# Kernel tuning notes

Measured on AMD Instinct MI355X. Metric: run time of the kernel, lower is better.

The kernel has to match this reference:

```python
import jax, jax.numpy as jnp
import numpy as np

B, S, HID = 2, 1024, 4096
NH, NKV = 32, 8            # query heads, kv heads (GQA)
D = HID // NH              # head_size = 128
G = NH // NKV              # groups = 4
SCALE = D ** -0.5


def setup_inputs() -> dict:
    key = jax.random.key(0)
    k1, k2, k3 = jax.random.split(key, 3)
    hidden_states = jax.random.normal(k1, (B, S, HID), dtype=jnp.float32)
    # rotary tables: dim=head_size, base=10000 (PositionRotaryEmbedding.static)
    inv_freq = 1.0 / (10000.0 ** (jnp.arange(0, D, 2, dtype=jnp.float32) / D))  # [D/2]
    t = jnp.arange(S, dtype=jnp.float32)
    freqs = jnp.outer(t, inv_freq)                       # [S, D/2]
    cos, sin = jnp.cos(freqs), jnp.sin(freqs)
    wqkv = jax.random.normal(k2, (HID, (NH + 2 * NKV) * D), dtype=jnp.float32) * (HID ** -0.5)
    wo = jax.random.normal(k3, (NH * D, HID), dtype=jnp.float32) * (HID ** -0.5)
    return {"hidden_states": hidden_states, "cos": cos, "sin": sin, "wqkv": wqkv, "wo": wo}


def _rope(x, cos, sin):
    # interleaved-pair rotary (TGI convention); x: [B,S,H,D], cos/sin: [S,D/2]
    x1, x2 = x[..., 0::2], x[..., 1::2]
    c = cos[None, :, None, :]
    s = sin[None, :, None, :]
    r1 = x1 * c - x2 * s
    r2 = x1 * s + x2 * c
    return jnp.stack([r1, r2], axis=-1).reshape(x.shape)


def reference(hidden_states, cos, sin, wqkv, wo):
    qkv = hidden_states @ wqkv                                  # [B,S,(NH+2*NKV)*D]
    q = qkv[..., : NH * D].reshape(B, S, NH, D)
    k = qkv[..., NH * D : (NH + NKV) * D].reshape(B, S, NKV, D)
    v = qkv[..., (NH + NKV) * D :].reshape(B, S, NKV, D)
    q = _rope(q, cos, sin)
    k = _rope(k, cos, sin)
    # GQA: group query heads over kv heads
    qg = q.reshape(B, S, NKV, G, D)
    scores = jnp.einsum('bqkgd,bskd->bkgqs', qg, k) * SCALE     # [B,NKV,G,S,S]
    causal = jnp.tril(jnp.ones((S, S), dtype=bool))
    scores = jnp.where(causal, scores, jnp.finfo(scores.dtype).min)
    p = jax.nn.softmax(scores, axis=-1)
    out = jnp.einsum('bkgqs,bskd->bqkgd', p, v).reshape(B, S, NH * D)
    return out @ wo                                             # [B,S,HID]
```

## Files before the change

kernel.cpp:

```cpp
#include <hip/hip_runtime.h>
#include <hip/hip_bf16.h>

typedef __bf16 bf16;
typedef __attribute__((ext_vector_type(2))) __bf16 bf16x2;
typedef __attribute__((ext_vector_type(4))) __bf16 bf16x4;
typedef __attribute__((ext_vector_type(8))) __bf16 bf16x8;
typedef __attribute__((ext_vector_type(4))) float f32x4;

#define NB 2
#define SEQ 1024
#define HIDN 4096
#define NH 32
#define NKV 8
#define DH 128
#define QKV_N 6144
static constexpr float SCALE = 0.08838834764831845f;

#define MFMA(a, b, c) __builtin_amdgcn_mfma_f32_16x16x32_bf16((a), (b), (c), 0, 0, 0)

__device__ __forceinline__ void async16(const void* g, void* l) {
  __builtin_amdgcn_global_load_lds(
      (const __attribute__((address_space(1))) unsigned int*)g,
      (__attribute__((address_space(3))) unsigned int*)l,
      16, 0, 0);
}

__device__ __forceinline__ void barrier_raw() {
  asm volatile("" ::: "memory");
  __builtin_amdgcn_s_barrier();
  asm volatile("" ::: "memory");
}
#define VMCNT(n) asm volatile("s_waitcnt vmcnt(" #n ")" ::: "memory")
#define LGKM0 asm volatile("s_waitcnt lgkmcnt(0)" ::: "memory")

__global__ __launch_bounds__(256) void cvt_f32_bf16(const float* __restrict__ src,
                                                    bf16* __restrict__ dst, int n4) {
  int i = blockIdx.x * 256 + threadIdx.x;
  if (i >= n4) return;
  const float4 v = ((const float4*)src)[i];
  bf16x4 o = {(bf16)v.x, (bf16)v.y, (bf16)v.z, (bf16)v.w};
  ((bf16x4*)dst)[i] = o;
}

__global__ __launch_bounds__(512) void transpose_cvt(const float* __restrict__ src,
                                                     bf16* __restrict__ dst, int R, int C) {
  __shared__ float tl[128][68];
  const int j0 = blockIdx.x * 64, i0 = blockIdx.y * 128;
  {
    const int r = threadIdx.x >> 2, c = (threadIdx.x & 3) * 16;
    const float* S = src + (size_t)(i0 + r) * C + j0 + c;
#pragma unroll
    for (int e = 0; e < 4; ++e) *(float4*)&tl[r][c + e * 4] = *(const float4*)&S[e * 4];
  }
  __syncthreads();
  {
    const int j = threadIdx.x >> 3, ic = (threadIdx.x & 7) * 16;
    bf16x8 o0, o1;
#pragma unroll
    for (int e = 0; e < 8; ++e) {
      o0[e] = (bf16)tl[ic + e][j];
      o1[e] = (bf16)tl[ic + 8 + e][j];
    }
    bf16* D = dst + (size_t)(j0 + j) * R + i0 + ic;
    *(bf16x8*)&D[0] = o0;
    *(bf16x8*)&D[8] = o1;
  }
}

__global__ __launch_bounds__(256) void vtrans(const bf16* __restrict__ src,
                                              bf16* __restrict__ dst) {
  __shared__ bf16 tl[64][72];
  const int bk = blockIdx.z;
  const int s0 = blockIdx.x * 64, d0 = blockIdx.y * 64;
  const bf16* S = src + ((size_t)bk * SEQ + s0) * DH + d0;
  bf16* D = dst + ((size_t)bk * DH + d0) * SEQ + s0;
  const int r = threadIdx.x >> 2, c = (threadIdx.x & 3) * 16;
  *(bf16x8*)&tl[r][c] = *(const bf16x8*)&S[(size_t)r * DH + c];
  *(bf16x8*)&tl[r][c + 8] = *(const bf16x8*)&S[(size_t)r * DH + c + 8];
  __syncthreads();
  bf16x8 o0, o1;
#pragma unroll
  for (int e = 0; e < 8; ++e) {
    o0[e] = tl[c + e][r];
    o1[e] = tl[c + 8 + e][r];
  }
  *(bf16x8*)&D[(size_t)r * SEQ + c] = o0;
  *(bf16x8*)&D[(size_t)r * SEQ + c + 8] = o1;
}

template <int BN, int MODE>
__global__ __launch_bounds__(512, 2) void gemm_dp(const bf16* __restrict__ A,
                                                  const bf16* __restrict__ BT,
                                                  void* __restrict__ Cout,
                                                  int N, int K,
                                                  const float* __restrict__ cosp,
                                                  const float* __restrict__ sinp,
                                                  bf16* __restrict__ Qo,
                                                  bf16* __restrict__ Ko,
                                                  bf16* __restrict__ Vo) {
  extern __shared__ char smem[];
  constexpr int CA = 128 * 32 * 2;
  constexpr int CB = BN * 32 * 2;
  constexpr int BUF = CA + CB;
  constexpr int LTOT = 1 + BN / 128;
  constexpr int FN = BN / 64;
  constexpr int FNH = FN / 2;
  const int t = threadIdx.x, lane = t & 63, w = t >> 6;
  const int l16 = lane & 15, lq = lane >> 4;
  const int wm = w >> 2, wn = w & 3;

  const int nwg = gridDim.x;
  const int lin = ((int)blockIdx.x & 7) * (nwg >> 3) + ((int)blockIdx.x >> 3);
  const int m0 = (lin & 15) * 128;
  const int n0 = (lin >> 4) * BN;

  const int sslot = (t & 3) ^ ((t >> 3) & 3);
  const bf16* gsrc[LTOT];
  gsrc[0] = A + (size_t)(m0 + (t >> 2)) * K + sslot * 8;
#pragma unroll
  for (int u = 1; u < LTOT; ++u)
    gsrc[u] = BT + (size_t)(n0 + (u - 1) * 128 + (t >> 2)) * K + sslot * 8;

  int abyte[4], bbyte[FN];
#pragma unroll
  for (int f = 0; f < 4; ++f) {
    const int r = wm * 64 + f * 16 + l16;
    abyte[f] = r * 64 + ((lq ^ ((r >> 1) & 3)) << 4);
  }
#pragma unroll
  for (int j = 0; j < FN; ++j) {
    const int r = wn * (BN / 4) + j * 16 + l16;
    bbyte[j] = CA + r * 64 + ((lq ^ ((r >> 1) & 3)) << 4);
  }

  auto stage_unit = [&](int kt, int u) {
    char* d = smem + (kt & 3) * BUF + u * 8192 + t * 16;
    async16(gsrc[u] + (size_t)kt * 32, d);
  };

  f32x4 acc[4][FN] = {};
  const int NT = K >> 5;

#pragma unroll
  for (int kt = 0; kt < 3; ++kt)
#pragma unroll
    for (int u = 0; u < LTOT; ++u) stage_unit(kt, u);
  if constexpr (LTOT == 4) { VMCNT(8); } else { VMCNT(6); }
  barrier_raw();

  for (int kt = 0; kt < NT; ++kt) {
    const char* buf = smem + (kt & 3) * BUF;
    const bool pf = (kt + 3 < NT);
    bf16x8 af[4], bf0[FNH];
#pragma unroll
    for (int f = 0; f < 4; ++f) af[f] = *(const bf16x8*)(buf + abyte[f]);
#pragma unroll
    for (int j = 0; j < FNH; ++j) bf0[j] = *(const bf16x8*)(buf + bbyte[j]);
    if (pf) {
      stage_unit(kt + 3, 0);
      stage_unit(kt + 3, 1);
    }
    barrier_raw();
    __builtin_amdgcn_s_setprio(1);
#pragma unroll
    for (int f = 0; f < 4; ++f)
#pragma unroll
      for (int j = 0; j < FNH; ++j) acc[f][j] = MFMA(af[f], bf0[j], acc[f][j]);
    __builtin_amdgcn_s_setprio(0);
    bf16x8 bf1[FN - FNH];
#pragma unroll
    for (int j = 0; j < FN - FNH; ++j) bf1[j] = *(const bf16x8*)(buf + bbyte[FNH + j]);
    if (pf) {
#pragma unroll
      for (int u = 2; u < LTOT; ++u) stage_unit(kt + 3, u);
    }
    if (pf) {
      if constexpr (LTOT == 4) { VMCNT(8); } else { VMCNT(6); }
    } else if (kt + 2 < NT) {
      if constexpr (LTOT == 4) { VMCNT(4); } else { VMCNT(3); }
    } else {
      VMCNT(0);
    }
    LGKM0;
    barrier_raw();
    __builtin_amdgcn_s_setprio(1);
#pragma unroll
    for (int f = 0; f < 4; ++f)
#pragma unroll
      for (int j = 0; j < FN - FNH; ++j)
        acc[f][FNH + j] = MFMA(af[f], bf1[j], acc[f][FNH + j]);
    __builtin_amdgcn_s_setprio(0);
  }

  if constexpr (MODE == 2) {
    LGKM0;
    barrier_raw();
    float* csl = (float*)smem;
    float* snl = (float*)(smem + 32768);
    const int s0 = m0 & 1023;
    const f32x4* cs = (const f32x4*)(cosp + s0 * 64);
    const f32x4* sn = (const f32x4*)(sinp + s0 * 64);
#pragma unroll
    for (int i = 0; i < 4; ++i) {
      ((f32x4*)csl)[t + i * 512] = cs[t + i * 512];
      ((f32x4*)snl)[t + i * 512] = sn[t + i * 512];
    }
    barrier_raw();
#pragma unroll
    for (int f = 0; f < 4; ++f)
#pragma unroll
      for (int j = 0; j < FN; ++j)
#pragma unroll
        for (int r = 0; r < 4; ++r) {
          const int row = m0 + wm * 64 + f * 16 + lq * 4 + r;
          const int col = n0 + wn * (BN / 4) + j * 16 + l16;
          const float v = acc[f][j][r];
          const float part = __shfl_xor(v, 1);
          const int bb = row >> 10, s = row & 1023;
          const int srel = wm * 64 + f * 16 + lq * 4 + r;
          if (col < 4096) {
            const int h = col >> 7, d = col & 127;
            const float c = csl[srel * 64 + (d >> 1)];
            const float sv = snl[srel * 64 + (d >> 1)];
            const float o = (l16 & 1) ? (part * sv + v * c) : (v * c - part * sv);
            Qo[((size_t)(bb * NH + h) * SEQ + s) * DH + d] = (bf16)(o * SCALE);
          } else if (col < 5120) {
            const int idx = col - 4096, kvh = idx >> 7, d = idx & 127;
            const float c = csl[srel * 64 + (d >> 1)];
            const float sv = snl[srel * 64 + (d >> 1)];
            const float o = (l16 & 1) ? (part * sv + v * c) : (v * c - part * sv);
            Ko[((size_t)(bb * NKV + kvh) * SEQ + s) * DH + d] = (bf16)o;
          } else {
            const int idx = col - 5120, kvh = idx >> 7, d = idx & 127;
            Vo[((size_t)(bb * NKV + kvh) * SEQ + s) * DH + d] = (bf16)v;
          }
        }
  } else {
#pragma unroll
    for (int f = 0; f < 4; ++f)
#pragma unroll
      for (int j = 0; j < FN; ++j)
#pragma unroll
        for (int r = 0; r < 4; ++r) {
          const int row = m0 + wm * 64 + f * 16 + lq * 4 + r;
          const int col = n0 + wn * (BN / 4) + j * 16 + l16;
          ((float*)Cout)[(size_t)row * N + col] = acc[f][j][r];
        }
  }
}

__global__ __launch_bounds__(512, 2) void flash_attn(const bf16* __restrict__ Q,
                                                     const bf16* __restrict__ K,
                                                     const bf16* __restrict__ VT,
                                                     bf16* __restrict__ O) {
  extern __shared__ char smem[];
  const int t = threadIdx.x, lane = t & 63, w = t >> 6;
  const int l16 = lane & 15, lq = lane >> 4;
  const int p = blockIdx.x;
  const int b = p >> 7, h = (p >> 2) & 31, Tb = p & 3;
  const int kvh = h >> 2;

  const bf16* Qb = Q + (size_t)(b * NH + h) * SEQ * DH;
  const bf16* Kb = K + (size_t)(b * NKV + kvh) * SEQ * DH;
  const bf16* Vb = VT + (size_t)(b * NKV + kvh) * DH * SEQ;

  const int qrA = Tb * 128 + w * 16;
  const int qrB = (7 - Tb) * 128 + w * 16;
  const int nAw = (qrA >> 6) + 1;
  const int nBw = (qrB >> 6) + 1;
  const int NT = 16 - 2 * Tb;

  bf16* plw = (bf16*)(smem + 98304) + w * (2 * 16 * 72);

  const bf16* kSrc = Kb + (size_t)(t >> 4) * DH + 8 * ((t & 15) ^ ((t >> 4) & 7));
  const bf16* vSrc = Vb + (size_t)(t >> 3) * SEQ + 8 * ((t & 7) ^ ((t >> 3) & 7));

  auto stage = [&](int kv) {
    char* bufb = smem + (kv % 3) * 32768;
    async16(kSrc + (size_t)(kv * 64) * DH, bufb + t * 16);
    async16(kSrc + (size_t)(kv * 64 + 32) * DH, bufb + 8192 + t * 16);
    async16(vSrc + kv * 64, bufb + 16384 + t * 16);
    async16(vSrc + (size_t)64 * SEQ + kv * 64, bufb + 24576 + t * 16);
  };

  int KX[4], VX[2];
#pragma unroll
  for (int kk = 0; kk < 4; ++kk) KX[kk] = ((kk * 4 + lq) ^ (l16 & 7)) << 4;
#pragma unroll
  for (int c = 0; c < 2; ++c) VX[c] = ((c * 4 + lq) ^ (l16 & 7)) << 4;

  bf16x8 qfA[4], qfB[4];
#pragma unroll
  for (int kk = 0; kk < 4; ++kk) {
    qfA[kk] = *(const bf16x8*)&Qb[(size_t)(qrA + l16) * DH + kk * 32 + lq * 8];
    qfB[kk] = *(const bf16x8*)&Qb[(size_t)(qrB + l16) * DH + kk * 32 + lq * 8];
  }

  f32x4 accA[8] = {}, accB[8] = {};
  float mA[4], lA[4], mB[4], lB[4];
#pragma unroll
  for (int r = 0; r < 4; ++r) {
    mA[r] = mB[r] = -INFINITY;
    lA[r] = lB[r] = 0.f;
  }

  auto finish = [&](f32x4(&s)[4], float(&m)[4], float(&l)[4], f32x4(&acc)[8], int slot,
                    bool mask, int kv, int qr) {
    if (mask) {
#pragma unroll
      for (int nt = 0; nt < 4; ++nt)
#pragma unroll
        for (int r = 0; r < 4; ++r)
          if (kv * 64 + nt * 16 + l16 > qr + lq * 4 + r) s[nt][r] = -INFINITY;
    }
#pragma unroll
    for (int r = 0; r < 4; ++r) {
      float mx = fmaxf(fmaxf(s[0][r], s[1][r]), fmaxf(s[2][r], s[3][r]));
#pragma unroll
      for (int off = 1; off < 16; off <<= 1) mx = fmaxf(mx, __shfl_xor(mx, off));
      const float mn = fmaxf(m[r], mx);
      const float corr = __expf(m[r] - mn);
      m[r] = mn;
      float ps = 0.f;
#pragma unroll
      for (int nt = 0; nt < 4; ++nt) {
        const float pv = __expf(s[nt][r] - mn);
        s[nt][r] = pv;
        ps += pv;
      }
#pragma unroll
      for (int off = 1; off < 16; off <<= 1) ps += __shfl_xor(ps, off);
      l[r] = l[r] * corr + ps;
#pragma unroll
      for (int j = 0; j < 8; ++j) acc[j][r] *= corr;
    }
#pragma unroll
    for (int nt = 0; nt < 4; ++nt)
#pragma unroll
      for (int r = 0; r < 4; ++r)
        plw[slot * 1152 + (lq * 4 + r) * 72 + nt * 16 + l16] = (bf16)s[nt][r];
  };

  stage(0);
  stage(1);
  VMCNT(4);
  barrier_raw();

  for (int kv = 0; kv < NT; ++kv) {
    const char* kbuf = smem + (kv % 3) * 32768;
    const char* vbuf = kbuf + 16384;
    if (kv + 2 < NT) stage(kv + 2);

    if (kv < nAw) {
      f32x4 sA[4] = {}, sB[4] = {};
      __builtin_amdgcn_s_setprio(1);
#pragma unroll
      for (int nt = 0; nt < 4; ++nt) {
        const char* kr = kbuf + (nt * 16 + l16) * 256;
        bf16x8 k0 = *(const bf16x8*)(kr + KX[0]);
        bf16x8 k1 = *(const bf16x8*)(kr + KX[1]);
        bf16x8 k2 = *(const bf16x8*)(kr + KX[2]);
        bf16x8 k3 = *(const bf16x8*)(kr + KX[3]);
        sA[nt] = MFMA(qfA[0], k0, sA[nt]);
        sB[nt] = MFMA(qfB[0], k0, sB[nt]);
        sA[nt] = MFMA(qfA[1], k1, sA[nt]);
        sB[nt] = MFMA(qfB[1], k1, sB[nt]);
        sA[nt] = MFMA(qfA[2], k2, sA[nt]);
        sB[nt] = MFMA(qfB[2], k2, sB[nt]);
        sA[nt] = MFMA(qfA[3], k3, sA[nt]);
        sB[nt] = MFMA(qfB[3], k3, sB[nt]);
      }
      __builtin_amdgcn_s_setprio(0);
      finish(sA, mA, lA, accA, 0, kv == nAw - 1, kv, qrA);
      finish(sB, mB, lB, accB, 1, kv == nBw - 1, kv, qrB);
      bf16x8 pA0 = *(const bf16x8*)&plw[l16 * 72 + lq * 8];
      bf16x8 pA1 = *(const bf16x8*)&plw[l16 * 72 + 32 + lq * 8];
      bf16x8 pB0 = *(const bf16x8*)&plw[1152 + l16 * 72 + lq * 8];
      bf16x8 pB1 = *(const bf16x8*)&plw[1152 + l16 * 72 + 32 + lq * 8];
      __builtin_amdgcn_s_setprio(1);
#pragma unroll
      for (int j = 0; j < 8; ++j) {
        const char* vr = vbuf + (j * 16 + l16) * 128;
        bf16x8 v0 = *(const bf16x8*)(vr + VX[0]);
        bf16x8 v1 = *(const bf16x8*)(vr + VX[1]);
        accA[j] = MFMA(pA0, v0, accA[j]);
        accB[j] = MFMA(pB0, v0, accB[j]);
        accA[j] = MFMA(pA1, v1, accA[j]);
        accB[j] = MFMA(pB1, v1, accB[j]);
      }
      __builtin_amdgcn_s_setprio(0);
    } else if (kv < nBw) {
      f32x4 sB[4] = {};
      __builtin_amdgcn_s_setprio(1);
#pragma unroll
      for (int nt = 0; nt < 4; ++nt) {
        const char* kr = kbuf + (nt * 16 + l16) * 256;
        bf16x8 k0 = *(const bf16x8*)(kr + KX[0]);
        bf16x8 k1 = *(const bf16x8*)(kr + KX[1]);
        bf16x8 k2 = *(const bf16x8*)(kr + KX[2]);
        bf16x8 k3 = *(const bf16x8*)(kr + KX[3]);
        sB[nt] = MFMA(qfB[0], k0, sB[nt]);
        sB[nt] = MFMA(qfB[1], k1, sB[nt]);
        sB[nt] = MFMA(qfB[2], k2, sB[nt]);
        sB[nt] = MFMA(qfB[3], k3, sB[nt]);
      }
      __builtin_amdgcn_s_setprio(0);
      finish(sB, mB, lB, accB, 1, kv == nBw - 1, kv, qrB);
      bf16x8 pB0 = *(const bf16x8*)&plw[1152 + l16 * 72 + lq * 8];
      bf16x8 pB1 = *(const bf16x8*)&plw[1152 + l16 * 72 + 32 + lq * 8];
      __builtin_amdgcn_s_setprio(1);
#pragma unroll
      for (int j = 0; j < 8; ++j) {
        const char* vr = vbuf + (j * 16 + l16) * 128;
        bf16x8 v0 = *(const bf16x8*)(vr + VX[0]);
        bf16x8 v1 = *(const bf16x8*)(vr + VX[1]);
        accB[j] = MFMA(pB0, v0, accB[j]);
        accB[j] = MFMA(pB1, v1, accB[j]);
      }
      __builtin_amdgcn_s_setprio(0);
    }

    if (kv + 2 < NT) { VMCNT(4); } else { VMCNT(0); }
    barrier_raw();
  }

  auto wout = [&](f32x4(&acc)[8], float(&l)[4], int qr) {
#pragma unroll
    for (int r = 0; r < 4; ++r) {
      const float inv = 1.f / l[r];
      const size_t orow = ((size_t)b * SEQ + qr + lq * 4 + r) * HIDN + h * DH;
#pragma unroll
      for (int j = 0; j < 8; ++j) O[orow + j * 16 + l16] = (bf16)(acc[j][r] * inv);
    }
  };
  wout(accA, lA, qrA);
  wout(accB, lB, qrB);
}

extern "C" void kernel_launch(void* const* d_in, const int* in_sizes, int n_in,
                              void* d_out, int out_size, void* d_ws, size_t ws_size,
                              hipStream_t stream) {
  const float* hidden = (const float*)d_in[0];
  const float* cosp = (const float*)d_in[1];
  const float* sinp = (const float*)d_in[2];
  const float* wqkv = (const float*)d_in[3];
  const float* wo = (const float*)d_in[4];
  float* out = (float*)d_out;

  char* ws = (char*)d_ws;
  bf16* hiddenB = (bf16*)(ws);
  bf16* wqkvT  = (bf16*)(ws + 16777216);
  bf16* woT    = (bf16*)(ws + 67108864);
  bf16* Vtmp   = (bf16*)(ws + 100663296);
  bf16* Qb     = (bf16*)(ws + 125829120);
  bf16* Kb     = (bf16*)(ws + 142606336);
  bf16* VTb    = (bf16*)(ws + 146800640);
  bf16* attnB  = hiddenB;

  cvt_f32_bf16<<<8192, 256, 0, stream>>>(hidden, hiddenB, 2097152);
  transpose_cvt<<<dim3(96, 32), 512, 0, stream>>>(wqkv, wqkvT, 4096, 6144);
  transpose_cvt<<<dim3(64, 32), 512, 0, stream>>>(wo, woT, 4096, 4096);
  gemm_dp<384, 2><<<dim3(256), 512, 131072, stream>>>(hiddenB, wqkvT, nullptr, 6144, 4096,
                                                      cosp, sinp, Qb, Kb, Vtmp);
  vtrans<<<dim3(16, 2, 16), 256, 0, stream>>>(Vtmp, VTb);
  flash_attn<<<dim3(256), 512, 135168, stream>>>(Qb, Kb, VTb, attnB);
  gemm_dp<256, 0><<<dim3(256), 512, 98304, stream>>>(attnB, woT, out, 4096, 4096,
                                                     nullptr, nullptr, nullptr, nullptr,
                                                     nullptr);
}
```

Measured before the change: 282.9 us.

## Add dedicated output-projection GEMM and lazy softmax rescaling in flash attention

```diff
diff --git a/kernel.cpp b/kernel.cpp
--- a/kernel.cpp
+++ b/kernel.cpp
@@ -249,6 +249,94 @@
   }
 }
 
+__global__ __launch_bounds__(512, 2) void gemm_h(const bf16* __restrict__ A,
+                                                 const bf16* __restrict__ BT,
+                                                 float* __restrict__ Cout,
+                                                 int N, int K) {
+  extern __shared__ char smem[];
+  constexpr int CA = 128 * 64 * 2;
+  constexpr int CB = 256 * 64 * 2;
+  constexpr int BUF = CA + CB;
+  const int t = threadIdx.x, lane = t & 63, w = t >> 6;
+  const int l16 = lane & 15, lq = lane >> 4;
+  const int wm = w >> 2, wn = w & 3;
+
+  const int nwg = gridDim.x;
+  const int lin = ((int)blockIdx.x & 7) * (nwg >> 3) + ((int)blockIdx.x >> 3);
+  const int m0 = (lin & 15) * 128;
+  const int n0 = (lin >> 4) * 256;
+
+  const int srow = t >> 3;
+  const int sslot = (t & 7) ^ (srow & 7);
+  const bf16* gsrc[6];
+  gsrc[0] = A + (size_t)(m0 + srow) * K + sslot * 8;
+  gsrc[1] = A + (size_t)(m0 + 64 + srow) * K + sslot * 8;
+#pragma unroll
+  for (int u = 2; u < 6; ++u)
+    gsrc[u] = BT + (size_t)(n0 + (u - 2) * 64 + srow) * K + sslot * 8;
+
+  int aoff[4], boff[4];
+#pragma unroll
+  for (int f = 0; f < 4; ++f) {
+    const int ra = wm * 64 + f * 16 + l16;
+    aoff[f] = ra * 128 + ((lq ^ (ra & 7)) << 4);
+    const int rb = wn * 64 + f * 16 + l16;
+    boff[f] = CA + rb * 128 + ((lq ^ (rb & 7)) << 4);
+  }
+
+  auto stage = [&](int kt) {
+    char* d = smem + (kt % 3) * BUF + t * 16;
+#pragma unroll
+    for (int u = 0; u < 6; ++u) async16(gsrc[u] + (size_t)kt * 64, d + u * 8192);
+  };
+
+  f32x4 acc[4][4] = {};
+  const int NT = K >> 6;
+
+  stage(0);
+  stage(1);
+  VMCNT(6);
+  barrier_raw();
+
+  for (int kt = 0; kt < NT; ++kt) {
+    const char* buf = smem + (kt % 3) * BUF;
+    if (kt + 2 < NT) stage(kt + 2);
+#pragma unroll
+    for (int kk = 0; kk < 2; ++kk) {
+      const int kx = kk * 64;
+      bf16x8 af[4], bfr[4];
+#pragma unroll
+      for (int f = 0; f < 4; ++f) af[f] = *(const bf16x8*)(buf + (aoff[f] ^ kx));
+#pragma unroll
+      for (int j = 0; j < 4; ++j) bfr[j] = *(const bf16x8*)(buf + (boff[j] ^ kx));
+      __builtin_amdgcn_s_setprio(1);
+#pragma unroll
+      for (int f = 0; f < 4; ++f)
+#pragma unroll
+        for (int j = 0; j < 4; ++j) acc[f][j] = MFMA(af[f], bfr[j], acc[f][j]);
+      __builtin_amdgcn_s_setprio(0);
+    }
+    if (kt + 2 < NT) {
+      VMCNT(6);
+    } else if (kt + 1 < NT) {
+      VMCNT(0);
+    }
+    LGKM0;
+    barrier_raw();
+  }
+
+#pragma unroll
+  for (int f = 0; f < 4; ++f)
+#pragma unroll
+    for (int j = 0; j < 4; ++j)
+#pragma unroll
+      for (int r = 0; r < 4; ++r) {
+        const int row = m0 + wm * 64 + f * 16 + lq * 4 + r;
+        const int col = n0 + wn * 64 + j * 16 + l16;
+        Cout[(size_t)row * N + col] = acc[f][j][r];
+      }
+}
+
 __global__ __launch_bounds__(512, 2) void flash_attn(const bf16* __restrict__ Q,
                                                      const bf16* __restrict__ K,
                                                      const bf16* __restrict__ VT,
@@ -318,21 +406,24 @@
       float mx = fmaxf(fmaxf(s[0][r], s[1][r]), fmaxf(s[2][r], s[3][r]));
 #pragma unroll
       for (int off = 1; off < 16; off <<= 1) mx = fmaxf(mx, __shfl_xor(mx, off));
-      const float mn = fmaxf(m[r], mx);
-      const float corr = __expf(m[r] - mn);
-      m[r] = mn;
+      if (__any(mx - m[r] > 8.f)) {
+        const float mn = fmaxf(m[r], mx);
+        const float corr = __expf(m[r] - mn);
+        m[r] = mn;
+        l[r] *= corr;
+#pragma unroll
+        for (int j = 0; j < 8; ++j) acc[j][r] *= corr;
+      }
       float ps = 0.f;
 #pragma unroll
       for (int nt = 0; nt < 4; ++nt) {
-        const float pv = __expf(s[nt][r] - mn);
+        const float pv = __expf(s[nt][r] - m[r]);
         s[nt][r] = pv;
         ps += pv;
       }
 #pragma unroll
       for (int off = 1; off < 16; off <<= 1) ps += __shfl_xor(ps, off);
-      l[r] = l[r] * corr + ps;
-#pragma unroll
-      for (int j = 0; j < 8; ++j) acc[j][r] *= corr;
+      l[r] += ps;
     }
 #pragma unroll
     for (int nt = 0; nt < 4; ++nt)
@@ -464,7 +555,5 @@
                                                       cosp, sinp, Qb, Kb, Vtmp);
   vtrans<<<dim3(16, 2, 16), 256, 0, stream>>>(Vtmp, VTb);
   flash_attn<<<dim3(256), 512, 135168, stream>>>(Qb, Kb, VTb, attnB);
-  gemm_dp<256, 0><<<dim3(256), 512, 98304, stream>>>(attnB, woT, out, 4096, 4096,
-                                                     nullptr, nullptr, nullptr, nullptr,
-                                                     nullptr);
-}
+  gemm_h<<<dim3(256), 512, 147456, stream>>>(attnB, woT, out, 4096, 4096);
+}
```

Result: slower. 313.7 us (+10.9%).
